# Kernel optimization log

Measured on AMD Instinct MI355X. Metric: run time of the kernel, lower is better.

Reference implementation:

```python
import jax, jax.numpy as jnp
import numpy as np

N, C, D, K = 4096, 512, 64, 10  # samples, clusters (c_max), feature_dim, num_classes
KAPPA_N = 10.0


def setup_inputs() -> dict:
    key = jax.random.key(0)
    k1, k2, k3, k4, k5, k6 = jax.random.split(key, 6)
    data = jax.random.normal(k1, (N, D), dtype=jnp.float32)
    labels = jax.random.randint(k2, (N,), 0, K)
    # cluster support counts n >= kappa_n (mature clusters)
    n = jax.random.uniform(k3, (C,), dtype=jnp.float32) * 90.0 + KAPPA_N
    mu = jax.random.normal(k4, (C, D), dtype=jnp.float32) * 2.0
    # S is the scatter matrix; covariance Sigma = S / n must be SPD, so
    # build S = n * (0.1 * A A^T + 0.5 I)
    A = jax.random.normal(k5, (C, D, D), dtype=jnp.float32)
    AAT = jnp.einsum('cij,ckj->cik', A, A) / D
    S = n[:, None, None] * (0.1 * AAT + 0.5 * jnp.eye(D, dtype=jnp.float32))
    # one-hot class label per cluster
    cls = jax.random.randint(k6, (C,), 0, K)
    cluster_labels = jax.nn.one_hot(cls, K, dtype=jnp.int32)
    return {"data": data, "labels": labels, "n": n, "mu": mu, "S": S,
            "cluster_labels": cluster_labels}


def reference(data, labels, n, mu, S, cluster_labels):
    # Inference path of eGAUSSp.forward: for each sample z,
    #   Gamma_j = exp(-0.5 * (z - mu_j)^T (S_j / n_j)^{-1} (z - mu_j))   (all c clusters)
    #   scores  = defuzzify = sum_j Gamma_j * onehot(label_j) / sum_j Gamma_j
    # Vectorized over the batch (no cross-sample dependence in eval mode).
    eps = jnp.asarray(1e-6, data.dtype)
    Sigma = S / n[:, None, None] + eps * jnp.eye(S.shape[-1], dtype=data.dtype)  # [C,D,D]
    Sinv = jnp.linalg.inv(Sigma)                                                  # [C,D,D]
    diff = data[:, None, :] - mu[None, :, :]          # [N,C,D]
    tmp = jnp.einsum('ncd,cde->nce', diff, Sinv)      # [N,C,D]
    d2 = jnp.einsum('nce,nce->nc', tmp, diff)         # [N,C] squared Mahalanobis
    Gamma = jnp.exp(-0.5 * d2)                        # [N,C] activations
    lab_f = cluster_labels.astype(data.dtype)         # [C,K]
    scores = (Gamma @ lab_f) / (jnp.sum(Gamma, axis=1, keepdims=True) + 1e-12)  # [N,K]
    pred = jnp.argmax(scores, axis=1)
    clusters = jnp.argmax(Gamma, axis=1)
    return scores, pred, clusters
```

## Files before the change

kernel.cpp:

```cpp
#include <hip/hip_runtime.h>
#include <hip/hip_bf16.h>
#include <math.h>

#define NS 4096
#define NC 512
#define ND 64
#define NK 10
#define NPAIR 2080
#define KP 2176
#define BOFF 2080
#define KOFF 2144
#define KSPLIT 4
#define KT_PER (KP / 32 / KSPLIT)
#define ZB 1024

typedef __attribute__((ext_vector_type(8))) short short8;
typedef __attribute__((ext_vector_type(4))) float floatx4;

__device__ inline unsigned short f2b(float x) {
    __hip_bfloat16 h = __float2bfloat16(x);
    return __builtin_bit_cast(unsigned short, h);
}
__device__ inline float b2f(unsigned short u) {
    __hip_bfloat16 h = __builtin_bit_cast(__hip_bfloat16, u);
    return __bfloat162float(h);
}

__device__ inline float rlane(float v, int k) {
    return __builtin_bit_cast(float, __builtin_amdgcn_readlane(__builtin_bit_cast(int, v), k));
}

__device__ inline void gl16(const void* g, void* l) {
    __builtin_amdgcn_global_load_lds(
        (const __attribute__((address_space(1))) unsigned int*)g,
        (__attribute__((address_space(3))) unsigned int*)l, 16, 0, 0);
}

__global__ void table_kernel(int2* __restrict__ edt) {
    const int e = threadIdx.x;
    int off = e * 64 - (e * (e - 1)) / 2;
    for (int d = e; d < 64; ++d) edt[off + d - e] = make_int2(e, d);
    edt[BOFF + e] = make_int2(e, 64);
    if (e == 0) edt[KOFF] = make_int2(64, 64);
    if (e < KP - KOFF - 1) edt[KOFF + 1 + e] = make_int2(65, 65);
}

__global__ __launch_bounds__(256, 4) void prep_kernel(
    const float* __restrict__ S, const float* __restrict__ n,
    const float* __restrict__ mu, const int* __restrict__ clab,
    const int2* __restrict__ edt, unsigned short* __restrict__ Bph,
    unsigned short* __restrict__ Bpl, float* __restrict__ d2,
    float* __restrict__ labf)
{
    __shared__ float AcolS[ND * (ND + 1)];
    __shared__ float cbuf[ND];
    __shared__ float rowbuf[2][ND];
    __shared__ float kksS[1];

    if (blockIdx.x >= NC) {
        const size_t base = (size_t)(blockIdx.x - NC) * 2048 + threadIdx.x * 8;
        *(float4*)&d2[base]     = make_float4(0.f, 0.f, 0.f, 0.f);
        *(float4*)&d2[base + 4] = make_float4(0.f, 0.f, 0.f, 0.f);
        return;
    }

    const int c = blockIdx.x;
    const int tid = threadIdx.x;
    const int j = tid & 63;
    const int w = tid >> 6;
    const int rbase = w * 16;

    const float inv_nc = 1.0f / n[c];
    const float* __restrict__ Sc = S + (size_t)c * ND * ND + j;

    float4 B0, B1, B2, B3;
#define LOADR(u) {                                                   \
    const float x0 = Sc[(rbase + 4*(u) + 0) * ND] * inv_nc;          \
    const float x1 = Sc[(rbase + 4*(u) + 1) * ND] * inv_nc;          \
    const float x2 = Sc[(rbase + 4*(u) + 2) * ND] * inv_nc;         \
    const float x3 = Sc[(rbase + 4*(u) + 3) * ND] * inv_nc;          \
    B##u.x = (rbase + 4*(u) + 0 == j) ? x0 + 1e-6f : x0;             \
    B##u.y = (rbase + 4*(u) + 1 == j) ? x1 + 1e-6f : x1;             \
    B##u.z = (rbase + 4*(u) + 2 == j) ? x2 + 1e-6f : x2;             \
    B##u.w = (rbase + 4*(u) + 3 == j) ? x3 + 1e-6f : x3; }
    LOADR(0) LOADR(1) LOADR(2) LOADR(3)
#undef LOADR

#define UPD4(u, K) {                                                  \
    const float c0 = rlane(B##u.x, K);                                \
    const float c1 = rlane(B##u.y, K);                                \
    const float c2 = rlane(B##u.z, K);                                \
    const float c3 = rlane(B##u.w, K);                                \
    B##u.x = (om && (4*(u)+0 == ((K)&15))) ? rowk : B##u.x * am - c0 * rowk; \
    B##u.y = (om && (4*(u)+1 == ((K)&15))) ? rowk : B##u.y * am - c1 * rowk; \
    B##u.z = (om && (4*(u)+2 == ((K)&15))) ? rowk : B##u.z * am - c2 * rowk; \
    B##u.w = (om && (4*(u)+3 == ((K)&15))) ? rowk : B##u.w * am - c3 * rowk; \
}
#define STEPC(TL, C, K) {                                             \
    if (w == ((K) >> 4)) {                                            \
        const float rp = B##TL.C;          \
        const float pv = rlane(rp, K);             \
        const float ip = 1.0f / pv;                                   \
        rowbuf[(K) & 1][j] = (j == (K)) ? ip : rp * ip;               \
    }                                                                 \
    __syncthreads();                                                  \
    const float rowk = rowbuf[(K) & 1][j];                            \
    const float am = (j == (K)) ? 0.0f : 1.0f;                        \
    const bool om = (w == ((K) >> 4));                                \
    UPD4(0, K) UPD4(1, K) UPD4(2, K) UPD4(3, K)                       \
}
#define STEP4(T, TL) STEPC(TL, x, 4*(T)+0) STEPC(TL, y, 4*(T)+1) \
                     STEPC(TL, z, 4*(T)+2) STEPC(TL, w, 4*(T)+3)
#define FOR16P(M) M(0,0) M(1,1) M(2,2) M(3,3) M(4,0) M(5,1) M(6,2) M(7,3) \
                  M(8,0) M(9,1) M(10,2) M(11,3) M(12,0) M(13,1) M(14,2) M(15,3)
    FOR16P(STEP4)
#undef FOR16P
#undef STEP4
#undef STEPC
#undef UPD4

#define MIR(u) *(float4*)&AcolS[j * (ND + 1) + rbase + 4*(u)] = B##u;
    MIR(0) MIR(1) MIR(2) MIR(3)
#undef MIR
    __syncthreads();

    if (w == 0) {
        const float* __restrict__ muc = mu + (size_t)c * ND;
        float y = 0.f;
        #pragma unroll
        for (int t = 0; t < 16; ++t) {
            const float4 v = *(const float4*)&AcolS[j * (ND + 1) + 4 * t];
            y += v.x * muc[4*t]     + v.y * muc[4*t + 1]
               + v.z * muc[4*t + 2] + v.w * muc[4*t + 3];
        }
        cbuf[j] = -2.0f * y;
        float kk = muc[j] * y;
        #pragma unroll
        for (int off = 32; off > 0; off >>= 1) kk += __shfl_down(kk, off);
        if (j == 0) {
            kksS[0] = kk;
            int lab = 0;
            for (int q = 0; q < NK; ++q) if (clab[c * NK + q] != 0) lab = q;
            labf[c] = (float)lab;
        }
    }
    __syncthreads();
    const float kks = kksS[0];

    unsigned short* __restrict__ ph = Bph + (size_t)c * KP;
    unsigned short* __restrict__ pl = Bpl + (size_t)c * KP;
    #pragma unroll
    for (int i = 0; i < 9; ++i) {
        const int t = w + 4 * i;
        if (t < KP / 64) {
            const int p = t * 64 + j;
            float val;
            if (p < NPAIR) {
                const int2 ed = edt[p];
                val = (ed.x == ed.y) ? AcolS[ed.x * (ND + 1) + ed.x]
                    : (AcolS[ed.y * (ND + 1) + ed.x] + AcolS[ed.x * (ND + 1) + ed.y]);
            } else if (p < KOFF) val = cbuf[p - BOFF];
            else if (p == KOFF)  val = kks;
            else                 val = 0.f;
            const unsigned short h = f2b(val);
            const unsigned short l = f2b(val - b2f(h));
            ph[p] = h;
            pl[p] = l;
        }
    }
}

__global__ __launch_bounds__(256, 2) void gemm_kernel(
    const float* __restrict__ data, const int2* __restrict__ edt,
    const unsigned short* __restrict__ Bph, const unsigned short* __restrict__ Bpl,
    float* __restrict__ d2)
{
    __shared__ float zS[64 * 68];
    __shared__ unsigned short AhS[64 * 40], AlS[64 * 40];
    __shared__ unsigned short BhS[256 * 32], BlS[256 * 32];

    const int tid  = threadIdx.x;
    const int lane = tid & 63, w = tid >> 6;
    const int quad = lane >> 4, rlo = lane & 15;
    const int m0 = blockIdx.x * 64;
    const int n0 = blockIdx.y * 256;
    const int koff0 = blockIdx.z * KT_PER * 32;

    #pragma unroll
    for (int q = 0; q < 4; ++q) {
        const int f = q * 256 + tid;
        const int r = f >> 4, c4 = f & 15;
        const float4 v = *(const float4*)&data[(size_t)(m0 + r) * ND + c4 * 4];
        *(float4*)&zS[r * 68 + c4 * 4] = v;
    }
    if (tid < 64) { zS[tid * 68 + 64] = 1.0f; zS[tid * 68 + 65] = 0.0f; }

    const int brow = tid >> 2, bseg = tid & 3;
    const int sseg = bseg ^ ((brow >> 2) & 3);
    const unsigned short* bGh[4];
    const unsigned short* bGl[4];
    unsigned short* bLh[4];
    unsigned short* bLl[4];
    #pragma unroll
    for (int rd = 0; rd < 4; ++rd) {
        const size_t off = (size_t)(n0 + rd * 64 + brow) * KP + sseg * 8 + koff0;
        bGh[rd] = Bph + off;
        bGl[rd] = Bpl + off;
        bLh[rd] = BhS + (rd * 256 + tid) * 8;
        bLl[rd] = BlS + (rd * 256 + tid) * 8;
    }

    const int jc = (tid & 15) * 2;
    const int rb = (tid >> 4) * 4;
    const int bswz = (quad ^ ((rlo >> 2) & 3)) * 8;

    floatx4 acc[4][4] = {};
    __syncthreads();

    for (int kt = 0; kt < KT_PER; ++kt) {
        const int ko = kt * 32;
        if (kt) __syncthreads();
        #pragma unroll
        for (int rd = 0; rd < 4; ++rd) {
            gl16(bGh[rd] + ko, bLh[rd]);
            gl16(bGl[rd] + ko, bLl[rd]);
        }
        const int2 ed0 = edt[koff0 + ko + jc];
        const int2 ed1 = edt[koff0 + ko + jc + 1];
        #pragma unroll
        for (int rr = 0; rr < 4; ++rr) {
            const int r = rb + rr;
            const float* zr = &zS[r * 68];
            const float v0 = zr[ed0.x] * zr[ed0.y];
            const float v1 = zr[ed1.x] * zr[ed1.y];
            const unsigned short h0 = f2b(v0), h1 = f2b(v1);
            const unsigned short l0 = f2b(v0 - b2f(h0)), l1 = f2b(v1 - b2f(h1));
            *(unsigned*)&AhS[r * 40 + jc] = (unsigned)h0 | ((unsigned)h1 << 16);
            *(unsigned*)&AlS[r * 40 + jc] = (unsigned)l0 | ((unsigned)l1 << 16);
        }
        __syncthreads();

        short8 ah[4], al[4], bh[4], bl[4];
        #pragma unroll
        for (int i = 0; i < 4; ++i) {
            ah[i] = *(const short8*)&AhS[(i * 16 + rlo) * 40 + quad * 8];
            al[i] = *(const short8*)&AlS[(i * 16 + rlo) * 40 + quad * 8];
        }
        #pragma unroll
        for (int j2 = 0; j2 < 4; ++j2) {
            const int r = w * 64 + j2 * 16 + rlo;
            bh[j2] = *(const short8*)&BhS[r * 32 + bswz];
            bl[j2] = *(const short8*)&BlS[r * 32 + bswz];
        }
        #pragma unroll
        for (int i = 0; i < 4; ++i)
            #pragma unroll
            for (int j2 = 0; j2 < 4; ++j2) {
                acc[i][j2] = __builtin_amdgcn_mfma_f32_16x16x32_bf16(al[i], bh[j2], acc[i][j2], 0, 0, 0);
                acc[i][j2] = __builtin_amdgcn_mfma_f32_16x16x32_bf16(ah[i], bl[j2], acc[i][j2], 0, 0, 0);
                acc[i][j2] = __builtin_amdgcn_mfma_f32_16x16x32_bf16(ah[i], bh[j2], acc[i][j2], 0, 0, 0);
            }
    }

    #pragma unroll
    for (int i = 0; i < 4; ++i)
        #pragma unroll
        for (int j2 = 0; j2 < 4; ++j2) {
            const int m = m0 + i * 16 + quad * 4;
            const int nn = n0 + w * 64 + j2 * 16 + rlo;
            #pragma unroll
            for (int r = 0; r < 4; ++r)
                atomicAdd(&d2[(size_t)(m + r) * NC + nn], acc[i][j2][r]);
        }
}

__global__ __launch_bounds__(256) void score_kernel(
    const float* __restrict__ d2, const float* __restrict__ labf,
    float* __restrict__ out)
{
    const int s = blockIdx.x * 4 + (threadIdx.x >> 6);
    const int l = threadIdx.x & 63;

    float numer[NK];
    #pragma unroll
    for (int q = 0; q < NK; ++q) numer[q] = 0.f;
    float denom = 0.f, gmax = -1.f;
    int gidx = 0;

    #pragma unroll
    for (int i = 0; i < NC / 256; ++i) {
        const int c0 = i * 256 + l * 4;
        const float4 v = *(const float4*)&d2[(size_t)s * NC + c0];
        #pragma unroll
        for (int r = 0; r < 4; ++r) {
            const int c = c0 + r;
            const float G = __expf(-0.5f * ((const float*)&v)[r]);
            denom += G;
            const int lab = (int)labf[c];
            #pragma unroll
            for (int q = 0; q < NK; ++q) numer[q] += (q == lab) ? G : 0.f;
            if (G > gmax) { gmax = G; gidx = c; }
        }
    }

    #pragma unroll
    for (int off = 32; off > 0; off >>= 1) {
        const float og = __shfl_down(gmax, off);
        const int   oi = __shfl_down(gidx, off);
        if (og > gmax || (og == gmax && oi < gidx)) { gmax = og; gidx = oi; }
        denom += __shfl_down(denom, off);
        #pragma unroll
        for (int q = 0; q < NK; ++q) numer[q] += __shfl_down(numer[q], off);
    }

    if (l == 0) {
        const float inv = 1.0f / (denom + 1e-12f);
        float best = -1.f; int pk = 0;
        #pragma unroll
        for (int q = 0; q < NK; ++q) {
            const float sc = numer[q] * inv;
            out[(size_t)s * NK + q] = sc;
            if (sc > best) { best = sc; pk = q; }
        }
        out[(size_t)NS * NK + s]      = (float)pk;
        out[(size_t)NS * NK + NS + s] = (float)gidx;
    }
}

extern "C" void kernel_launch(void* const* d_in, const int* in_sizes, int n_in,
                              void* d_out, int out_size, void* d_ws, size_t ws_size,
                              hipStream_t stream)
{
    const float* data = (const float*)d_in[0];
    const float* n    = (const float*)d_in[2];
    const float* mu   = (const float*)d_in[3];
    const float* S    = (const float*)d_in[4];
    const int*   clab = (const int*)d_in[5];

    char* w = (char*)d_ws;
    int2* edt = (int2*)(w);
    unsigned short* Bph = (unsigned short*)(w + 35651584);
    unsigned short* Bpl = (unsigned short*)(w + 37879808);
    float* d2   = (float*)(w + 40108032);
    float* labf = (float*)(w + 48496640);

    hipLaunchKernelGGL(table_kernel, dim3(1), dim3(64), 0, stream, edt);
    hipLaunchKernelGGL(prep_kernel,  dim3(NC + ZB), dim3(256), 0, stream,
                       S, n, mu, clab, edt, Bph, Bpl, d2, labf);
    hipLaunchKernelGGL(gemm_kernel,  dim3(NS / 64, NC / 256, KSPLIT), dim3(256), 0, stream,
                       data, edt, Bph, Bpl, d2);
    hipLaunchKernelGGL(score_kernel, dim3(NS / 4), dim3(256), 0, stream,
                       d2, labf, (float*)d_out);
}
```

Baseline: 154.3 us.

## Precompute quadratic feature rows in prep and double-buffer GEMM loads

The per-sample quadratic feature vector (z_i*z_j pairs, split into bf16 hi/lo) is now built once in extra prep_kernel blocks and written to global memory. Previously every GEMM block rebuilt it for each k-tile. The GEMM kernel then loads both A and B tiles with async global-to-LDS copies into double-buffered shared memory, so the next tile's loads overlap the current MFMAs. The edge table is shrunk to uchar2. In exchange, the Q matrices add roughly 35 MB of global writes and reads, and the shared-memory footprint grows.

```diff
diff --git a/kernel.cpp b/kernel.cpp
--- a/kernel.cpp
+++ b/kernel.cpp
@@ -13,6 +13,7 @@
 #define KSPLIT 4
 #define KT_PER (KP / 32 / KSPLIT)
 #define ZB 1024
+#define QB 2048
 
 typedef __attribute__((ext_vector_type(8))) short short8;
 typedef __attribute__((ext_vector_type(4))) float floatx4;
@@ -36,26 +37,52 @@
         (__attribute__((address_space(3))) unsigned int*)l, 16, 0, 0);
 }
 
-__global__ void table_kernel(int2* __restrict__ edt) {
+__global__ void table_kernel(uchar2* __restrict__ edt) {
     const int e = threadIdx.x;
     int off = e * 64 - (e * (e - 1)) / 2;
-    for (int d = e; d < 64; ++d) edt[off + d - e] = make_int2(e, d);
-    edt[BOFF + e] = make_int2(e, 64);
-    if (e == 0) edt[KOFF] = make_int2(64, 64);
-    if (e < KP - KOFF - 1) edt[KOFF + 1 + e] = make_int2(65, 65);
+    for (int d = e; d < 64; ++d) edt[off + d - e] = make_uchar2(e, d);
+    edt[BOFF + e] = make_uchar2(e, 64);
+    if (e == 0) edt[KOFF] = make_uchar2(64, 64);
+    if (e < KP - KOFF - 1) edt[KOFF + 1 + e] = make_uchar2(65, 65);
 }
 
 __global__ __launch_bounds__(256, 4) void prep_kernel(
-    const float* __restrict__ S, const float* __restrict__ n,
-    const float* __restrict__ mu, const int* __restrict__ clab,
-    const int2* __restrict__ edt, unsigned short* __restrict__ Bph,
-    unsigned short* __restrict__ Bpl, float* __restrict__ d2,
-    float* __restrict__ labf)
+    const float* __restrict__ data, const float* __restrict__ S,
+    const float* __restrict__ n, const float* __restrict__ mu,
+    const int* __restrict__ clab, const uchar2* __restrict__ edt,
+    unsigned short* __restrict__ Qh, unsigned short* __restrict__ Ql,
+    unsigned short* __restrict__ Bph, unsigned short* __restrict__ Bpl,
+    float* __restrict__ d2, float* __restrict__ labf)
 {
     __shared__ float AcolS[ND * (ND + 1)];
     __shared__ float cbuf[ND];
     __shared__ float rowbuf[2][ND];
     __shared__ float kksS[1];
+    __shared__ float zq[2][66];
+
+    if (blockIdx.x >= NC + ZB) {
+        const int qb = blockIdx.x - (NC + ZB);
+        const int half = threadIdx.x >> 7;
+        const int i = threadIdx.x & 127;
+        const int row = qb * 2 + half;
+        if (i < 64) zq[half][i] = data[(size_t)row * ND + i];
+        else if (i == 64) { zq[half][64] = 1.0f; zq[half][65] = 0.0f; }
+        __syncthreads();
+        const float* __restrict__ zr = zq[half];
+        unsigned short* __restrict__ qh = Qh + (size_t)row * KP;
+        unsigned short* __restrict__ ql = Ql + (size_t)row * KP;
+        #pragma unroll
+        for (int t = 0; t < 17; ++t) {
+            const int p = t * 128 + i;
+            const uchar2 ed = edt[p];
+            const float v = zr[ed.x] * zr[ed.y];
+            const unsigned short h = f2b(v);
+            const unsigned short l = f2b(v - b2f(h));
+            qh[p] = h;
+            ql[p] = l;
+        }
+        return;
+    }
 
     if (blockIdx.x >= NC) {
         const size_t base = (size_t)(blockIdx.x - NC) * 2048 + threadIdx.x * 8;
@@ -77,7 +104,7 @@
 #define LOADR(u) {                                                   \
     const float x0 = Sc[(rbase + 4*(u) + 0) * ND] * inv_nc;          \
     const float x1 = Sc[(rbase + 4*(u) + 1) * ND] * inv_nc;          \
-    const float x2 = Sc[(rbase + 4*(u) + 2) * ND] * inv_nc;         \
+    const float x2 = Sc[(rbase + 4*(u) + 2) * ND] * inv_nc;          \
     const float x3 = Sc[(rbase + 4*(u) + 3) * ND] * inv_nc;          \
     B##u.x = (rbase + 4*(u) + 0 == j) ? x0 + 1e-6f : x0;             \
     B##u.y = (rbase + 4*(u) + 1 == j) ? x1 + 1e-6f : x1;             \
@@ -156,7 +183,7 @@
             const int p = t * 64 + j;
             float val;
             if (p < NPAIR) {
-                const int2 ed = edt[p];
+                const uchar2 ed = edt[p];
                 val = (ed.x == ed.y) ? AcolS[ed.x * (ND + 1) + ed.x]
                     : (AcolS[ed.y * (ND + 1) + ed.x] + AcolS[ed.x * (ND + 1) + ed.y]);
             } else if (p < KOFF) val = cbuf[p - BOFF];
@@ -171,13 +198,12 @@
 }
 
 __global__ __launch_bounds__(256, 2) void gemm_kernel(
-    const float* __restrict__ data, const int2* __restrict__ edt,
+    const unsigned short* __restrict__ Qh, const unsigned short* __restrict__ Ql,
     const unsigned short* __restrict__ Bph, const unsigned short* __restrict__ Bpl,
     float* __restrict__ d2)
 {
-    __shared__ float zS[64 * 68];
-    __shared__ unsigned short AhS[64 * 40], AlS[64 * 40];
-    __shared__ unsigned short BhS[256 * 32], BlS[256 * 32];
+    __shared__ unsigned short AhS[2][64 * 32], AlS[2][64 * 32];
+    __shared__ unsigned short BhS[2][256 * 32], BlS[2][256 * 32];
 
     const int tid  = threadIdx.x;
     const int lane = tid & 63, w = tid >> 6;
@@ -186,72 +212,57 @@
     const int n0 = blockIdx.y * 256;
     const int koff0 = blockIdx.z * KT_PER * 32;
 
-    #pragma unroll
-    for (int q = 0; q < 4; ++q) {
-        const int f = q * 256 + tid;
-        const int r = f >> 4, c4 = f & 15;
-        const float4 v = *(const float4*)&data[(size_t)(m0 + r) * ND + c4 * 4];
-        *(float4*)&zS[r * 68 + c4 * 4] = v;
-    }
-    if (tid < 64) { zS[tid * 68 + 64] = 1.0f; zS[tid * 68 + 65] = 0.0f; }
-
-    const int brow = tid >> 2, bseg = tid & 3;
-    const int sseg = bseg ^ ((brow >> 2) & 3);
+    const int srow = tid >> 2;
+    const int sswz = (tid & 3) ^ ((srow >> 2) & 3);
+    const unsigned short* aGh = Qh + (size_t)(m0 + srow) * KP + koff0 + sswz * 8;
+    const unsigned short* aGl = Ql + (size_t)(m0 + srow) * KP + koff0 + sswz * 8;
     const unsigned short* bGh[4];
     const unsigned short* bGl[4];
-    unsigned short* bLh[4];
-    unsigned short* bLl[4];
     #pragma unroll
     for (int rd = 0; rd < 4; ++rd) {
-        const size_t off = (size_t)(n0 + rd * 64 + brow) * KP + sseg * 8 + koff0;
+        const size_t off = (size_t)(n0 + rd * 64 + srow) * KP + koff0 + sswz * 8;
         bGh[rd] = Bph + off;
         bGl[rd] = Bpl + off;
-        bLh[rd] = BhS + (rd * 256 + tid) * 8;
-        bLl[rd] = BlS + (rd * 256 + tid) * 8;
-    }
-
-    const int jc = (tid & 15) * 2;
-    const int rb = (tid >> 4) * 4;
-    const int bswz = (quad ^ ((rlo >> 2) & 3)) * 8;
+    }
+    const int swz8 = (quad ^ ((rlo >> 2) & 3)) * 8;
 
     floatx4 acc[4][4] = {};
+
+    gl16(aGh, &AhS[0][tid * 8]);
+    gl16(aGl, &AlS[0][tid * 8]);
+    #pragma unroll
+    for (int rd = 0; rd < 4; ++rd) {
+        gl16(bGh[rd], &BhS[0][(rd * 256 + tid) * 8]);
+        gl16(bGl[rd], &BlS[0][(rd * 256 + tid) * 8]);
+    }
     __syncthreads();
 
+    int cur = 0;
     for (int kt = 0; kt < KT_PER; ++kt) {
-        const int ko = kt * 32;
-        if (kt) __syncthreads();
-        #pragma unroll
-        for (int rd = 0; rd < 4; ++rd) {
-            gl16(bGh[rd] + ko, bLh[rd]);
-            gl16(bGl[rd] + ko, bLl[rd]);
-        }
-        const int2 ed0 = edt[koff0 + ko + jc];
-        const int2 ed1 = edt[koff0 + ko + jc + 1];
-        #pragma unroll
-        for (int rr = 0; rr < 4; ++rr) {
-            const int r = rb + rr;
-            const float* zr = &zS[r * 68];
-            const float v0 = zr[ed0.x] * zr[ed0.y];
-            const float v1 = zr[ed1.x] * zr[ed1.y];
-            const unsigned short h0 = f2b(v0), h1 = f2b(v1);
-            const unsigned short l0 = f2b(v0 - b2f(h0)), l1 = f2b(v1 - b2f(h1));
-            *(unsigned*)&AhS[r * 40 + jc] = (unsigned)h0 | ((unsigned)h1 << 16);
-            *(unsigned*)&AlS[r * 40 + jc] = (unsigned)l0 | ((unsigned)l1 << 16);
-        }
-        __syncthreads();
+        if (kt + 1 < KT_PER) {
+            const int ko = (kt + 1) * 32;
+            gl16(aGh + ko, &AhS[cur ^ 1][tid * 8]);
+            gl16(aGl + ko, &AlS[cur ^ 1][tid * 8]);
+            #pragma unroll
+            for (int rd = 0; rd < 4; ++rd) {
+                gl16(bGh[rd] + ko, &BhS[cur ^ 1][(rd * 256 + tid) * 8]);
+                gl16(bGl[rd] + ko, &BlS[cur ^ 1][(rd * 256 + tid) * 8]);
+            }
+        }
 
         short8 ah[4], al[4], bh[4], bl[4];
         #pragma unroll
         for (int i = 0; i < 4; ++i) {
-            ah[i] = *(const short8*)&AhS[(i * 16 + rlo) * 40 + quad * 8];
-            al[i] = *(const short8*)&AlS[(i * 16 + rlo) * 40 + quad * 8];
+            ah[i] = *(const short8*)&AhS[cur][(i * 16 + rlo) * 32 + swz8];
+            al[i] = *(const short8*)&AlS[cur][(i * 16 + rlo) * 32 + swz8];
         }
         #pragma unroll
         for (int j2 = 0; j2 < 4; ++j2) {
             const int r = w * 64 + j2 * 16 + rlo;
-            bh[j2] = *(const short8*)&BhS[r * 32 + bswz];
-            bl[j2] = *(const short8*)&BlS[r * 32 + bswz];
-        }
+            bh[j2] = *(const short8*)&BhS[cur][r * 32 + swz8];
+            bl[j2] = *(const short8*)&BlS[cur][r * 32 + swz8];
+        }
+
         #pragma unroll
         for (int i = 0; i < 4; ++i)
             #pragma unroll
@@ -260,6 +271,9 @@
                 acc[i][j2] = __builtin_amdgcn_mfma_f32_16x16x32_bf16(ah[i], bl[j2], acc[i][j2], 0, 0, 0);
                 acc[i][j2] = __builtin_amdgcn_mfma_f32_16x16x32_bf16(ah[i], bh[j2], acc[i][j2], 0, 0, 0);
             }
+
+        __syncthreads();
+        cur ^= 1;
     }
 
     #pragma unroll
@@ -338,17 +352,19 @@
     const int*   clab = (const int*)d_in[5];
 
     char* w = (char*)d_ws;
-    int2* edt = (int2*)(w);
+    unsigned short* Qh  = (unsigned short*)(w);
+    unsigned short* Ql  = (unsigned short*)(w + 17825792);
     unsigned short* Bph = (unsigned short*)(w + 35651584);
     unsigned short* Bpl = (unsigned short*)(w + 37879808);
     float* d2   = (float*)(w + 40108032);
     float* labf = (float*)(w + 48496640);
+    uchar2* edt = (uchar2*)(w + 48498688);
 
     hipLaunchKernelGGL(table_kernel, dim3(1), dim3(64), 0, stream, edt);
-    hipLaunchKernelGGL(prep_kernel,  dim3(NC + ZB), dim3(256), 0, stream,
-                       S, n, mu, clab, edt, Bph, Bpl, d2, labf);
+    hipLaunchKernelGGL(prep_kernel,  dim3(NC + ZB + QB), dim3(256), 0, stream,
+                       data, S, n, mu, clab, edt, Qh, Ql, Bph, Bpl, d2, labf);
     hipLaunchKernelGGL(gemm_kernel,  dim3(NS / 64, NC / 256, KSPLIT), dim3(256), 0, stream,
-                       data, edt, Bph, Bpl, d2);
+                       Qh, Ql, Bph, Bpl, d2);
     hipLaunchKernelGGL(score_kernel, dim3(NS / 4), dim3(256), 0, stream,
                        d2, labf, (float*)d_out);
 }
```

Measured after the change: 154.0 us. Within noise of the previous version (-0.2%).
